# Optimization experiments

Hardware: AMD Instinct MI355X
Metric: run time of the kernel (lower is better)

## Reference

```python
import jax, jax.numpy as jnp
import numpy as np

B, S, F = 4, 2048, 512
H, DK, DV, FILT = 8, 64, 64, 512

def setup_inputs() -> dict:
    key = jax.random.key(0)
    ks = jax.random.split(key, 11)
    sc_in = 1.0 / np.sqrt(F)
    sc_o = 1.0 / np.sqrt(H * DV)
    return {
        "x_q": jax.random.normal(ks[0], (B, S, F), jnp.float32),
        "x_k": jax.random.normal(ks[1], (B, S, F), jnp.float32),
        "x_v": jax.random.normal(ks[2], (B, S, F), jnp.float32),
        "Wq": jax.random.normal(ks[3], (H, F, DK), jnp.float32) * sc_in,
        "bq": jax.random.normal(ks[4], (H, DK), jnp.float32) * 0.01,
        "Wk": jax.random.normal(ks[5], (H, F, DK), jnp.float32) * sc_in,
        "bk": jax.random.normal(ks[6], (H, DK), jnp.float32) * 0.01,
        "Wv": jax.random.normal(ks[7], (H, F, DV), jnp.float32) * sc_in,
        "bv": jax.random.normal(ks[8], (H, DV), jnp.float32) * 0.01,
        "Wo": jax.random.normal(ks[9], (H * DV, FILT), jnp.float32) * sc_o,
        "bo": jax.random.normal(ks[10], (FILT,), jnp.float32) * 0.01,
    }

def reference(x_q, x_k, x_v, Wq, bq, Wk, bk, Wv, bv, Wo, bo):
    d_k = Wq.shape[-1]
    # per-head Dense projections, batched over heads: [B,H,S,dk/dv]
    q = jnp.einsum("bsf,hfk->bhsk", x_q, Wq) + bq[:, None, :]
    k = jnp.einsum("bsf,hfk->bhsk", x_k, Wk) + bk[:, None, :]
    v = jnp.einsum("bsf,hfv->bhsv", x_v, Wv) + bv[:, None, :]
    # scaled dot-product attention (scale by 1/sqrt(d_k) as in map_fn)
    scores = jnp.einsum("bhsk,bhtk->bhst", q, k) / jnp.sqrt(jnp.asarray(d_k, q.dtype))
    attn = jax.nn.softmax(scores, axis=-1)
    out = jnp.einsum("bhst,bhtv->bhsv", attn, v)
    # concat heads along feature dim -> [B,S,H*DV], then output linear
    bsz, h, s, dv = out.shape
    concat = out.transpose(0, 2, 1, 3).reshape(bsz, s, h * dv)
    return concat @ Wo + bo
```

## Files before the change

kernel.cpp:

```cpp
#include <hip/hip_runtime.h>

#define B_    4
#define S_    2048
#define H_    8
#define M_    (B_ * S_)

typedef __bf16    bf16_t;
typedef _Float16  f16_t;
typedef __bf16   bf16x8 __attribute__((ext_vector_type(8)));
typedef __bf16   bf16x4 __attribute__((ext_vector_type(4)));
typedef _Float16 f16x8  __attribute__((ext_vector_type(8)));
typedef float    f32x16 __attribute__((ext_vector_type(16)));

union B8 { uint4 u; bf16x8 v; bf16_t e[8]; };
union B4 { uint2 u; bf16x4 v; bf16_t e[4]; };
union H8 { uint4 u; f16x8  v; f16_t  e[8]; };
union H4 { uint2 u; f16_t  e[4]; };

#define QSCALE 0.1803368801111204f

__global__ __launch_bounds__(256) void convert_weights(
    const float* __restrict__ w0, const float* __restrict__ w1,
    const float* __restrict__ w2, const float* __restrict__ wo,
    bf16_t* __restrict__ t0, bf16_t* __restrict__ t1,
    bf16_t* __restrict__ t2, f16_t* __restrict__ wot)
{
    __shared__ float T[64][65];
    const int z   = blockIdx.z;
    const int k0  = blockIdx.x * 64;
    const int tid = threadIdx.x;
    const int row = tid & 63, q4 = tid >> 6;

    if (z < 3) {
        const float* W  = z == 0 ? w0 : z == 1 ? w1 : w2;
        bf16_t*      Wt = z == 0 ? t0 : z == 1 ? t1 : t2;
        const int h = blockIdx.y;
        const float* Wh = W + (size_t)h * 512 * 64;
        #pragma unroll
        for (int i = 0; i < 4; ++i) {
            int fq = q4 * 4 + i;
            float4 v = *(const float4*)(Wh + (size_t)(k0 + row) * 64 + fq * 4);
            T[row][fq * 4 + 0] = v.x; T[row][fq * 4 + 1] = v.y;
            T[row][fq * 4 + 2] = v.z; T[row][fq * 4 + 3] = v.w;
        }
        __syncthreads();
        bf16_t* Wth = Wt + (size_t)h * 64 * 512;
        #pragma unroll
        for (int i = 0; i < 4; ++i) {
            int kq = q4 * 4 + i;
            B4 o;
            #pragma unroll
            for (int j = 0; j < 4; ++j) o.e[j] = (bf16_t)T[kq * 4 + j][row];
            *(uint2*)(Wth + (size_t)row * 512 + k0 + kq * 4) = o.u;
        }
    } else {
        const int n0 = blockIdx.y * 64;
        #pragma unroll
        for (int i = 0; i < 4; ++i) {
            int fq = q4 * 4 + i;
            float4 v = *(const float4*)(wo + (size_t)(k0 + row) * 512 + n0 + fq * 4);
            T[row][fq * 4 + 0] = v.x; T[row][fq * 4 + 1] = v.y;
            T[row][fq * 4 + 2] = v.z; T[row][fq * 4 + 3] = v.w;
        }
        __syncthreads();
        #pragma unroll
        for (int i = 0; i < 4; ++i) {
            int kq = q4 * 4 + i;
            H4 o;
            #pragma unroll
            for (int j = 0; j < 4; ++j) o.e[j] = (f16_t)T[kq * 4 + j][row];
            *(uint2*)(wot + (size_t)(n0 + row) * 512 + k0 + kq * 4) = o.u;
        }
    }
}

__global__ __launch_bounds__(256) void proj_tiled(
    const float* __restrict__ xq, const float* __restrict__ xk,
    const float* __restrict__ xv,
    const bf16_t* __restrict__ Wtq, const bf16_t* __restrict__ Wtk,
    const bf16_t* __restrict__ Wtv,
    const float* __restrict__ bq, const float* __restrict__ bk,
    const float* __restrict__ bv,
    bf16_t* __restrict__ Qb, bf16_t* __restrict__ Kb, bf16_t* __restrict__ Vt)
{
    __shared__ bf16_t As[128 * 72];
    __shared__ bf16_t Bs[128 * 72];

    const int z = blockIdx.z;
    const float*  X    = z == 0 ? xq  : z == 1 ? xk  : xv;
    const bf16_t* Wt   = z == 0 ? Wtq : z == 1 ? Wtk : Wtv;
    const float*  bias = z == 0 ? bq  : z == 1 ? bk  : bv;

    const int tid  = threadIdx.x;
    const int wave = tid >> 6, lane = tid & 63;
    const int l31  = lane & 31, half = lane >> 5;
    const int m0   = blockIdx.x * 128;
    const int n0   = blockIdx.y * 128;
    const int mw   = (wave & 1) * 64;
    const int nw   = (wave >> 1) * 64;

    const int sr = tid >> 1;
    const int sc = (tid & 1) * 32;

    float4 ra0[4], ra1[4];
    uint4  rb[4];
    {
        const float*  ap = X  + (size_t)(m0 + sr) * 512 + sc;
        const bf16_t* bp = Wt + (size_t)(n0 + sr) * 512 + sc;
        #pragma unroll
        for (int i = 0; i < 4; ++i) {
            ra0[i] = *(const float4*)(ap + i * 8);
            ra1[i] = *(const float4*)(ap + i * 8 + 4);
            rb[i]  = *(const uint4*)(bp + i * 8);
        }
    }

    f32x16 acc[2][2];
    #pragma unroll
    for (int mt = 0; mt < 2; ++mt)
        #pragma unroll
        for (int nt = 0; nt < 2; ++nt)
            #pragma unroll
            for (int i = 0; i < 16; ++i) acc[mt][nt][i] = 0.0f;

    for (int k0 = 0; k0 < 512; k0 += 64) {
        __syncthreads();
        #pragma unroll
        for (int i = 0; i < 4; ++i) {
            B8 w;
            w.e[0] = (bf16_t)ra0[i].x; w.e[1] = (bf16_t)ra0[i].y;
            w.e[2] = (bf16_t)ra0[i].z; w.e[3] = (bf16_t)ra0[i].w;
            w.e[4] = (bf16_t)ra1[i].x; w.e[5] = (bf16_t)ra1[i].y;
            w.e[6] = (bf16_t)ra1[i].z; w.e[7] = (bf16_t)ra1[i].w;
            *(uint4*)&As[sr * 72 + sc + i * 8] = w.u;
            *(uint4*)&Bs[sr * 72 + sc + i * 8] = rb[i];
        }
        __syncthreads();
        if (k0 + 64 < 512) {
            const float*  ap = X  + (size_t)(m0 + sr) * 512 + k0 + 64 + sc;
            const bf16_t* bp = Wt + (size_t)(n0 + sr) * 512 + k0 + 64 + sc;
            #pragma unroll
            for (int i = 0; i < 4; ++i) {
                ra0[i] = *(const float4*)(ap + i * 8);
                ra1[i] = *(const float4*)(ap + i * 8 + 4);
                rb[i]  = *(const uint4*)(bp + i * 8);
            }
        }

        #pragma unroll
        for (int kc = 0; kc < 4; ++kc) {
            B8 a0, a1, b0, b1;
            a0.u = *(const uint4*)&As[(mw + l31)      * 72 + kc * 16 + half * 8];
            a1.u = *(const uint4*)&As[(mw + 32 + l31) * 72 + kc * 16 + half * 8];
            b0.u = *(const uint4*)&Bs[(nw + l31)      * 72 + kc * 16 + half * 8];
            b1.u = *(const uint4*)&Bs[(nw + 32 + l31) * 72 + kc * 16 + half * 8];
            acc[0][0] = __builtin_amdgcn_mfma_f32_32x32x16_bf16(a0.v, b0.v, acc[0][0], 0, 0, 0);
            acc[0][1] = __builtin_amdgcn_mfma_f32_32x32x16_bf16(a0.v, b1.v, acc[0][1], 0, 0, 0);
            acc[1][0] = __builtin_amdgcn_mfma_f32_32x32x16_bf16(a1.v, b0.v, acc[1][0], 0, 0, 0);
            acc[1][1] = __builtin_amdgcn_mfma_f32_32x32x16_bf16(a1.v, b1.v, acc[1][1], 0, 0, 0);
        }
    }

    if (z <= 1) {
        const float sc_ = (z == 0) ? QSCALE : 1.0f;
        bf16_t* Out = (z == 0) ? Qb : Kb;
        #pragma unroll
        for (int mt = 0; mt < 2; ++mt)
            #pragma unroll
            for (int nt = 0; nt < 2; ++nt) {
                int n = n0 + nw + nt * 32 + l31;
                float bv_ = bias[n];
                #pragma unroll
                for (int r = 0; r < 16; ++r) {
                    int m = m0 + mw + mt * 32 + (r & 3) + 8 * (r >> 2) + 4 * half;
                    Out[(size_t)m * 512 + n] = (bf16_t)((acc[mt][nt][r] + bv_) * sc_);
                }
            }
    } else {
        const int b  = m0 >> 11;
        const int sb = (m0 & 2047);
        #pragma unroll
        for (int mt = 0; mt < 2; ++mt)
            #pragma unroll
            for (int nt = 0; nt < 2; ++nt) {
                int n = n0 + nw + nt * 32 + l31;
                float bv_ = bias[n];
                int h = n >> 6, d = n & 63;
                bf16_t* base = Vt + ((size_t)(b * 8 + h) * 64 + d) * 2048 + sb + mw + mt * 32;
                #pragma unroll
                for (int g = 0; g < 4; ++g) {
                    B4 p;
                    #pragma unroll
                    for (int j = 0; j < 4; ++j) p.e[j] = (bf16_t)(acc[mt][nt][g * 4 + j] + bv_);
                    *(uint2*)(base + 8 * g + 4 * half) = p.u;
                }
            }
    }
}

__global__ __launch_bounds__(512) void attn_mfma(
    const bf16_t* __restrict__ Q, const bf16_t* __restrict__ K,
    const bf16_t* __restrict__ Vt, f16_t* __restrict__ O)
{
    __shared__ char smraw[36864];
    bf16_t* KsBuf = (bf16_t*)smraw;
    bf16_t* VsBuf = KsBuf + 2 * 64 * 72;

    const int bh  = blockIdx.y;
    const int b   = bh >> 3, h = bh & 7;
    const int q0  = blockIdx.x * 128;
    const int tid = threadIdx.x;
    const int wave = tid >> 6, lane = tid & 63;
    const int l31 = lane & 31, half = lane >> 5;
    const int qsub = wave & 3, ksplit = wave >> 2;

    bf16x8 qf[4];
    {
        const bf16_t* qp = Q + ((size_t)(b * S_ + q0 + qsub * 32 + l31)) * 512 + h * 64 + half * 8;
        #pragma unroll
        for (int ks = 0; ks < 4; ++ks) {
            B8 t; t.u = *(const uint4*)(qp + ks * 16);
            qf[ks] = t.v;
        }
    }

    f32x16 o0, o1;
    #pragma unroll
    for (int i = 0; i < 16; ++i) { o0[i] = 0.0f; o1[i] = 0.0f; }
    float l_i = 0.0f;

    const bf16_t* Kbase = K + ((size_t)b * S_) * 512 + h * 64;
    const bf16_t* Vbase = Vt + ((size_t)bh * 64) * 2048;

    const int sbuf = tid >> 8;
    const int p    = tid & 255;
    const int kr = p >> 3, kc8 = p & 7;
    const int vd = p >> 2, vj = p & 3;
    const int kqmap[4] = {0, 2, 1, 3};
    const int vkq = kqmap[vj];
    bf16_t* KsS = KsBuf + sbuf * (64 * 72);
    bf16_t* VsS = VsBuf + sbuf * (64 * 72);
    const bf16_t* KsC = KsBuf + ksplit * (64 * 72);
    const bf16_t* VsC = VsBuf + ksplit * (64 * 72);

    uint4 kreg0, kreg1;
    uint2 vreg[4];
    {
        const int tb = sbuf * 1024;
        kreg0 = *(const uint4*)(Kbase + (size_t)(tb + kr) * 512 + kc8 * 8);
        kreg1 = *(const uint4*)(Kbase + (size_t)(tb + kr + 32) * 512 + kc8 * 8);
        #pragma unroll
        for (int g = 0; g < 4; ++g)
            vreg[g] = *(const uint2*)(Vbase + (size_t)vd * 2048 + tb + g * 16 + vkq * 4);
    }

    for (int t0 = 0; t0 < 1024; t0 += 64) {
        __syncthreads();
        *(uint4*)&KsS[kr * 72 + kc8 * 8]        = kreg0;
        *(uint4*)&KsS[(kr + 32) * 72 + kc8 * 8] = kreg1;
        #pragma unroll
        for (int g = 0; g < 4; ++g)
            *(uint2*)&VsS[vd * 72 + g * 16 + vj * 4] = vreg[g];
        __syncthreads();

        if (t0 + 64 < 1024) {
            const int tb = sbuf * 1024 + t0 + 64;
            kreg0 = *(const uint4*)(Kbase + (size_t)(tb + kr) * 512 + kc8 * 8);
            kreg1 = *(const uint4*)(Kbase + (size_t)(tb + kr + 32) * 512 + kc8 * 8);
            #pragma unroll
            for (int g = 0; g < 4; ++g)
                vreg[g] = *(const uint2*)(Vbase + (size_t)vd * 2048 + tb + g * 16 + vkq * 4);
        }

        f32x16 s0, s1;
        #pragma unroll
        for (int i = 0; i < 16; ++i) { s0[i] = 0.0f; s1[i] = 0.0f; }
        #pragma unroll
        for (int ks = 0; ks < 4; ++ks) {
            B8 k0, k1;
            k0.u = *(const uint4*)(&KsC[l31 * 72 + ks * 16 + half * 8]);
            k1.u = *(const uint4*)(&KsC[(32 + l31) * 72 + ks * 16 + half * 8]);
            s0 = __builtin_amdgcn_mfma_f32_32x32x16_bf16(k0.v, qf[ks], s0, 0, 0, 0);
            s1 = __builtin_amdgcn_mfma_f32_32x32x16_bf16(k1.v, qf[ks], s1, 0, 0, 0);
        }

        float ls = 0.0f;
        #pragma unroll
        for (int r = 0; r < 16; ++r) {
            s0[r] = __builtin_amdgcn_exp2f(s0[r]); ls += s0[r];
            s1[r] = __builtin_amdgcn_exp2f(s1[r]); ls += s1[r];
        }
        l_i += ls;

        B8 pf[4];
        #pragma unroll
        for (int j = 0; j < 8; ++j) {
            pf[0].e[j] = (bf16_t)s0[j];
            pf[1].e[j] = (bf16_t)s0[8 + j];
            pf[2].e[j] = (bf16_t)s1[j];
            pf[3].e[j] = (bf16_t)s1[8 + j];
        }

        #pragma unroll
        for (int c = 0; c < 4; ++c) {
            B8 va, vb;
            va.u = *(const uint4*)(&VsC[l31 * 72 + c * 16 + half * 8]);
            vb.u = *(const uint4*)(&VsC[(32 + l31) * 72 + c * 16 + half * 8]);
            o0 = __builtin_amdgcn_mfma_f32_32x32x16_bf16(va.v, pf[c].v, o0, 0, 0, 0);
            o1 = __builtin_amdgcn_mfma_f32_32x32x16_bf16(vb.v, pf[c].v, o1, 0, 0, 0);
        }
    }

    l_i += __shfl_xor(l_i, 32);
    __syncthreads();
    float* co = (float*)smraw;
    float* cl = co + 4 * 32 * 68;
    if (ksplit == 1) {
        float* reg = co + qsub * (32 * 68);
        #pragma unroll
        for (int r = 0; r < 16; ++r) {
            reg[r * 68 + lane]        = o0[r];
            reg[(16 + r) * 68 + lane] = o1[r];
        }
        cl[qsub * 64 + lane] = l_i;
    }
    __syncthreads();
    if (ksplit == 0) {
        float* reg = co + qsub * (32 * 68);
        float inv = 1.0f / (l_i + cl[qsub * 64 + lane]);
        f16_t* Ob = O + ((size_t)(b * S_ + q0 + qsub * 32 + l31)) * 512 + h * 64;
        #pragma unroll
        for (int g = 0; g < 4; ++g) {
            H4 a, c;
            #pragma unroll
            for (int j = 0; j < 4; ++j) {
                int r = g * 4 + j;
                a.e[j] = (f16_t)((o0[r] + reg[r * 68 + lane]) * inv);
                c.e[j] = (f16_t)((o1[r] + reg[(16 + r) * 68 + lane]) * inv);
            }
            int d = 8 * g + 4 * half;
            *(uint2*)(Ob + d)      = a.u;
            *(uint2*)(Ob + 32 + d) = c.u;
        }
    }
}

__global__ __launch_bounds__(256) void gemm_out_tiled(
    const f16_t* __restrict__ A, const f16_t* __restrict__ Wot,
    const float* __restrict__ bias, float* __restrict__ C)
{
    __shared__ f16_t As[64 * 72];
    __shared__ f16_t Bs[64 * 72];

    const int tid  = threadIdx.x;
    const int wave = tid >> 6, lane = tid & 63;
    const int l31  = lane & 31, half = lane >> 5;
    const int m0   = blockIdx.x * 64;
    const int n0   = blockIdx.y * 64;
    const int mw   = (wave & 1) * 32;
    const int nw   = (wave >> 1) * 32;

    const int sr  = tid >> 2;
    const int so  = (tid & 3) * 16;

    uint4 pA0, pA1, pB0, pB1;
    {
        const f16_t* ap = A   + (size_t)(m0 + sr) * 512 + so;
        const f16_t* bp = Wot + (size_t)(n0 + sr) * 512 + so;
        pA0 = *(const uint4*)(ap); pA1 = *(const uint4*)(ap + 8);
        pB0 = *(const uint4*)(bp); pB1 = *(const uint4*)(bp + 8);
    }

    f32x16 acc;
    #pragma unroll
    for (int i = 0; i < 16; ++i) acc[i] = 0.0f;

    for (int k0 = 0; k0 < 512; k0 += 64) {
        __syncthreads();
        *(uint4*)&As[sr * 72 + so]     = pA0;
        *(uint4*)&As[sr * 72 + so + 8] = pA1;
        *(uint4*)&Bs[sr * 72 + so]     = pB0;
        *(uint4*)&Bs[sr * 72 + so + 8] = pB1;
        __syncthreads();
        if (k0 + 64 < 512) {
            const f16_t* ap = A   + (size_t)(m0 + sr) * 512 + k0 + 64 + so;
            const f16_t* bp = Wot + (size_t)(n0 + sr) * 512 + k0 + 64 + so;
            pA0 = *(const uint4*)(ap); pA1 = *(const uint4*)(ap + 8);
            pB0 = *(const uint4*)(bp); pB1 = *(const uint4*)(bp + 8);
        }

        #pragma unroll
        for (int kc = 0; kc < 4; ++kc) {
            H8 a, b;
            a.u = *(const uint4*)&As[(mw + l31) * 72 + kc * 16 + half * 8];
            b.u = *(const uint4*)&Bs[(nw + l31) * 72 + kc * 16 + half * 8];
            acc = __builtin_amdgcn_mfma_f32_32x32x16_f16(a.v, b.v, acc, 0, 0, 0);
        }
    }

    const int n = n0 + nw + l31;
    const float bias0 = bias[n];
    #pragma unroll
    for (int r = 0; r < 16; ++r) {
        int m = m0 + mw + (r & 3) + 8 * (r >> 2) + 4 * half;
        C[(size_t)m * 512 + n] = acc[r] + bias0;
    }
}

extern "C" void kernel_launch(void* const* d_in, const int* in_sizes, int n_in,
                              void* d_out, int out_size, void* d_ws, size_t ws_size,
                              hipStream_t stream)
{
    const float* x_q = (const float*)d_in[0];
    const float* x_k = (const float*)d_in[1];
    const float* x_v = (const float*)d_in[2];
    const float* Wq  = (const float*)d_in[3];
    const float* bq  = (const float*)d_in[4];
    const float* Wk  = (const float*)d_in[5];
    const float* bk  = (const float*)d_in[6];
    const float* Wv  = (const float*)d_in[7];
    const float* bv  = (const float*)d_in[8];
    const float* Wo  = (const float*)d_in[9];
    const float* bo  = (const float*)d_in[10];
    float* out = (float*)d_out;

    char* W = (char*)d_ws;
    bf16_t* Wtq = (bf16_t*)W;
    bf16_t* Wtk = Wtq + (size_t)8 * 64 * 512;
    bf16_t* Wtv = Wtk + (size_t)8 * 64 * 512;
    f16_t*  Wot = (f16_t*)(Wtv + (size_t)8 * 64 * 512);
    bf16_t* Qb  = (bf16_t*)(Wot + (size_t)512 * 512);
    bf16_t* Kb  = Qb + (size_t)M_ * 512;
    bf16_t* Vt  = Kb + (size_t)M_ * 512;
    f16_t*  AO  = (f16_t*)(Vt + (size_t)M_ * 512);

    convert_weights<<<dim3(8, 8, 4), 256, 0, stream>>>(
        Wq, Wk, Wv, Wo, Wtq, Wtk, Wtv, Wot);

    proj_tiled<<<dim3(64, 4, 3), 256, 0, stream>>>(
        x_q, x_k, x_v, Wtq, Wtk, Wtv, bq, bk, bv, Qb, Kb, Vt);

    attn_mfma<<<dim3(S_ / 128, B_ * H_), 512, 0, stream>>>(Qb, Kb, Vt, AO);

    gemm_out_tiled<<<dim3(128, 8), 256, 0, stream>>>(AO, Wot, bo, out);
}
```

Before: 214.5 us.

## Fuse weight transpose and conversion into projection and output GEMM loaders

Removes the separate convert_weights kernel and instead reads fp32 weights directly inside the projection and output GEMMs, converting to bf16/f16 in registers and scattering them transposed into shared memory. This saves a kernel launch and the workspace round trip for the converted weights. In exchange each GEMM block repeats the weight conversion, reads twice as many weight bytes as fp32, and does scalar 2-byte shared-memory stores that may bank-conflict. The pipeline was also reordered so the next-tile global loads are issued before the second barrier.

After: 223.5 us. 1.04x slower.

```diff
diff --git a/kernel.cpp b/kernel.cpp
--- a/kernel.cpp
+++ b/kernel.cpp
@@ -19,66 +19,20 @@
 
 #define QSCALE 0.1803368801111204f
 
-__global__ __launch_bounds__(256) void convert_weights(
-    const float* __restrict__ w0, const float* __restrict__ w1,
-    const float* __restrict__ w2, const float* __restrict__ wo,
-    bf16_t* __restrict__ t0, bf16_t* __restrict__ t1,
-    bf16_t* __restrict__ t2, f16_t* __restrict__ wot)
-{
-    __shared__ float T[64][65];
-    const int z   = blockIdx.z;
-    const int k0  = blockIdx.x * 64;
-    const int tid = threadIdx.x;
-    const int row = tid & 63, q4 = tid >> 6;
-
-    if (z < 3) {
-        const float* W  = z == 0 ? w0 : z == 1 ? w1 : w2;
-        bf16_t*      Wt = z == 0 ? t0 : z == 1 ? t1 : t2;
-        const int h = blockIdx.y;
-        const float* Wh = W + (size_t)h * 512 * 64;
-        #pragma unroll
-        for (int i = 0; i < 4; ++i) {
-            int fq = q4 * 4 + i;
-            float4 v = *(const float4*)(Wh + (size_t)(k0 + row) * 64 + fq * 4);
-            T[row][fq * 4 + 0] = v.x; T[row][fq * 4 + 1] = v.y;
-            T[row][fq * 4 + 2] = v.z; T[row][fq * 4 + 3] = v.w;
-        }
-        __syncthreads();
-        bf16_t* Wth = Wt + (size_t)h * 64 * 512;
-        #pragma unroll
-        for (int i = 0; i < 4; ++i) {
-            int kq = q4 * 4 + i;
-            B4 o;
-            #pragma unroll
-            for (int j = 0; j < 4; ++j) o.e[j] = (bf16_t)T[kq * 4 + j][row];
-            *(uint2*)(Wth + (size_t)row * 512 + k0 + kq * 4) = o.u;
-        }
-    } else {
-        const int n0 = blockIdx.y * 64;
-        #pragma unroll
-        for (int i = 0; i < 4; ++i) {
-            int fq = q4 * 4 + i;
-            float4 v = *(const float4*)(wo + (size_t)(k0 + row) * 512 + n0 + fq * 4);
-            T[row][fq * 4 + 0] = v.x; T[row][fq * 4 + 1] = v.y;
-            T[row][fq * 4 + 2] = v.z; T[row][fq * 4 + 3] = v.w;
-        }
-        __syncthreads();
-        #pragma unroll
-        for (int i = 0; i < 4; ++i) {
-            int kq = q4 * 4 + i;
-            H4 o;
-            #pragma unroll
-            for (int j = 0; j < 4; ++j) o.e[j] = (f16_t)T[kq * 4 + j][row];
-            *(uint2*)(wot + (size_t)(n0 + row) * 512 + k0 + kq * 4) = o.u;
-        }
-    }
+__device__ __forceinline__ uint4 pack_bf16x8(float4 a, float4 b) {
+    B8 w;
+    w.e[0] = (bf16_t)a.x; w.e[1] = (bf16_t)a.y;
+    w.e[2] = (bf16_t)a.z; w.e[3] = (bf16_t)a.w;
+    w.e[4] = (bf16_t)b.x; w.e[5] = (bf16_t)b.y;
+    w.e[6] = (bf16_t)b.z; w.e[7] = (bf16_t)b.w;
+    return w.u;
 }
 
 __global__ __launch_bounds__(256) void proj_tiled(
     const float* __restrict__ xq, const float* __restrict__ xk,
     const float* __restrict__ xv,
-    const bf16_t* __restrict__ Wtq, const bf16_t* __restrict__ Wtk,
-    const bf16_t* __restrict__ Wtv,
+    const float* __restrict__ Wq, const float* __restrict__ Wk,
+    const float* __restrict__ Wv,
     const float* __restrict__ bq, const float* __restrict__ bk,
     const float* __restrict__ bv,
     bf16_t* __restrict__ Qb, bf16_t* __restrict__ Kb, bf16_t* __restrict__ Vt)
@@ -87,9 +41,9 @@
     __shared__ bf16_t Bs[128 * 72];
 
     const int z = blockIdx.z;
-    const float*  X    = z == 0 ? xq  : z == 1 ? xk  : xv;
-    const bf16_t* Wt   = z == 0 ? Wtq : z == 1 ? Wtk : Wtv;
-    const float*  bias = z == 0 ? bq  : z == 1 ? bk  : bv;
+    const float* X    = z == 0 ? xq : z == 1 ? xk : xv;
+    const float* Wsrc = z == 0 ? Wq : z == 1 ? Wk : Wv;
+    const float* bias = z == 0 ? bq : z == 1 ? bk : bv;
 
     const int tid  = threadIdx.x;
     const int wave = tid >> 6, lane = tid & 63;
@@ -101,17 +55,35 @@
 
     const int sr = tid >> 1;
     const int sc = (tid & 1) * 32;
-
-    float4 ra0[4], ra1[4];
-    uint4  rb[4];
+    const int kk  = tid & 63;
+    const int oct = tid >> 6;
+    size_t wbase[4];
+    int    nloc[4];
+    #pragma unroll
+    for (int r4 = 0; r4 < 4; ++r4) {
+        int nl = (oct + r4 * 4) * 8;
+        nloc[r4] = nl;
+        int h = (n0 + nl) >> 6;
+        wbase[r4] = ((size_t)h * 512 + kk) * 64 + ((n0 + nl) & 63);
+    }
+
+    uint4 ab[4];
+    B4 pw0[4], pw1[4];
     {
-        const float*  ap = X  + (size_t)(m0 + sr) * 512 + sc;
-        const bf16_t* bp = Wt + (size_t)(n0 + sr) * 512 + sc;
-        #pragma unroll
-        for (int i = 0; i < 4; ++i) {
-            ra0[i] = *(const float4*)(ap + i * 8);
-            ra1[i] = *(const float4*)(ap + i * 8 + 4);
-            rb[i]  = *(const uint4*)(bp + i * 8);
+        const float* ap = X + (size_t)(m0 + sr) * 512 + sc;
+        #pragma unroll
+        for (int i = 0; i < 4; ++i)
+            ab[i] = pack_bf16x8(*(const float4*)(ap + i * 8),
+                                *(const float4*)(ap + i * 8 + 4));
+        #pragma unroll
+        for (int r4 = 0; r4 < 4; ++r4) {
+            const float* wp = Wsrc + wbase[r4];
+            float4 a = *(const float4*)(wp);
+            float4 b = *(const float4*)(wp + 4);
+            pw0[r4].e[0] = (bf16_t)a.x; pw0[r4].e[1] = (bf16_t)a.y;
+            pw0[r4].e[2] = (bf16_t)a.z; pw0[r4].e[3] = (bf16_t)a.w;
+            pw1[r4].e[0] = (bf16_t)b.x; pw1[r4].e[1] = (bf16_t)b.y;
+            pw1[r4].e[2] = (bf16_t)b.z; pw1[r4].e[3] = (bf16_t)b.w;
         }
     }
 
@@ -126,26 +98,34 @@
     for (int k0 = 0; k0 < 512; k0 += 64) {
         __syncthreads();
         #pragma unroll
-        for (int i = 0; i < 4; ++i) {
-            B8 w;
-            w.e[0] = (bf16_t)ra0[i].x; w.e[1] = (bf16_t)ra0[i].y;
-            w.e[2] = (bf16_t)ra0[i].z; w.e[3] = (bf16_t)ra0[i].w;
-            w.e[4] = (bf16_t)ra1[i].x; w.e[5] = (bf16_t)ra1[i].y;
-            w.e[6] = (bf16_t)ra1[i].z; w.e[7] = (bf16_t)ra1[i].w;
-            *(uint4*)&As[sr * 72 + sc + i * 8] = w.u;
-            *(uint4*)&Bs[sr * 72 + sc + i * 8] = rb[i];
-        }
-        __syncthreads();
+        for (int i = 0; i < 4; ++i)
+            *(uint4*)&As[sr * 72 + sc + i * 8] = ab[i];
+        #pragma unroll
+        for (int r4 = 0; r4 < 4; ++r4) {
+            #pragma unroll
+            for (int j = 0; j < 4; ++j) {
+                Bs[(nloc[r4] + j) * 72 + kk]     = pw0[r4].e[j];
+                Bs[(nloc[r4] + 4 + j) * 72 + kk] = pw1[r4].e[j];
+            }
+        }
         if (k0 + 64 < 512) {
-            const float*  ap = X  + (size_t)(m0 + sr) * 512 + k0 + 64 + sc;
-            const bf16_t* bp = Wt + (size_t)(n0 + sr) * 512 + k0 + 64 + sc;
-            #pragma unroll
-            for (int i = 0; i < 4; ++i) {
-                ra0[i] = *(const float4*)(ap + i * 8);
-                ra1[i] = *(const float4*)(ap + i * 8 + 4);
-                rb[i]  = *(const uint4*)(bp + i * 8);
-            }
-        }
+            const float* ap = X + (size_t)(m0 + sr) * 512 + k0 + 64 + sc;
+            #pragma unroll
+            for (int i = 0; i < 4; ++i)
+                ab[i] = pack_bf16x8(*(const float4*)(ap + i * 8),
+                                    *(const float4*)(ap + i * 8 + 4));
+            #pragma unroll
+            for (int r4 = 0; r4 < 4; ++r4) {
+                const float* wp = Wsrc + wbase[r4] + (size_t)(k0 + 64) * 64;
+                float4 a = *(const float4*)(wp);
+                float4 b = *(const float4*)(wp + 4);
+                pw0[r4].e[0] = (bf16_t)a.x; pw0[r4].e[1] = (bf16_t)a.y;
+                pw0[r4].e[2] = (bf16_t)a.z; pw0[r4].e[3] = (bf16_t)a.w;
+                pw1[r4].e[0] = (bf16_t)b.x; pw1[r4].e[1] = (bf16_t)b.y;
+                pw1[r4].e[2] = (bf16_t)b.z; pw1[r4].e[3] = (bf16_t)b.w;
+            }
+        }
+        __syncthreads();
 
         #pragma unroll
         for (int kc = 0; kc < 4; ++kc) {
@@ -346,7 +326,7 @@
 }
 
 __global__ __launch_bounds__(256) void gemm_out_tiled(
-    const f16_t* __restrict__ A, const f16_t* __restrict__ Wot,
+    const f16_t* __restrict__ A, const float* __restrict__ Wo,
     const float* __restrict__ bias, float* __restrict__ C)
 {
     __shared__ f16_t As[64 * 72];
@@ -360,15 +340,29 @@
     const int mw   = (wave & 1) * 32;
     const int nw   = (wave >> 1) * 32;
 
-    const int sr  = tid >> 2;
-    const int so  = (tid & 3) * 16;
-
-    uint4 pA0, pA1, pB0, pB1;
+    const int sr = tid >> 2;
+    const int so = (tid & 3) * 16;
+    const int kk  = tid & 63;
+    const int oct = tid >> 6;
+    int nloc[2];
+    nloc[0] = oct * 8;
+    nloc[1] = (oct + 4) * 8;
+
+    uint4 pA0, pA1;
+    H4 pw0[2], pw1[2];
     {
-        const f16_t* ap = A   + (size_t)(m0 + sr) * 512 + so;
-        const f16_t* bp = Wot + (size_t)(n0 + sr) * 512 + so;
+        const f16_t* ap = A + (size_t)(m0 + sr) * 512 + so;
         pA0 = *(const uint4*)(ap); pA1 = *(const uint4*)(ap + 8);
-        pB0 = *(const uint4*)(bp); pB1 = *(const uint4*)(bp + 8);
+        #pragma unroll
+        for (int r2 = 0; r2 < 2; ++r2) {
+            const float* wp = Wo + (size_t)kk * 512 + n0 + nloc[r2];
+            float4 a = *(const float4*)(wp);
+            float4 b = *(const float4*)(wp + 4);
+            pw0[r2].e[0] = (f16_t)a.x; pw0[r2].e[1] = (f16_t)a.y;
+            pw0[r2].e[2] = (f16_t)a.z; pw0[r2].e[3] = (f16_t)a.w;
+            pw1[r2].e[0] = (f16_t)b.x; pw1[r2].e[1] = (f16_t)b.y;
+            pw1[r2].e[2] = (f16_t)b.z; pw1[r2].e[3] = (f16_t)b.w;
+        }
     }
 
     f32x16 acc;
@@ -379,15 +373,29 @@
         __syncthreads();
         *(uint4*)&As[sr * 72 + so]     = pA0;
         *(uint4*)&As[sr * 72 + so + 8] = pA1;
-        *(uint4*)&Bs[sr * 72 + so]     = pB0;
-        *(uint4*)&Bs[sr * 72 + so + 8] = pB1;
-        __syncthreads();
+        #pragma unroll
+        for (int r2 = 0; r2 < 2; ++r2) {
+            #pragma unroll
+            for (int j = 0; j < 4; ++j) {
+                Bs[(nloc[r2] + j) * 72 + kk]     = pw0[r2].e[j];
+                Bs[(nloc[r2] + 4 + j) * 72 + kk] = pw1[r2].e[j];
+            }
+        }
         if (k0 + 64 < 512) {
-            const f16_t* ap = A   + (size_t)(m0 + sr) * 512 + k0 + 64 + so;
-            const f16_t* bp = Wot + (size_t)(n0 + sr) * 512 + k0 + 64 + so;
+            const f16_t* ap = A + (size_t)(m0 + sr) * 512 + k0 + 64 + so;
             pA0 = *(const uint4*)(ap); pA1 = *(const uint4*)(ap + 8);
-            pB0 = *(const uint4*)(bp); pB1 = *(const uint4*)(bp + 8);
-        }
+            #pragma unroll
+            for (int r2 = 0; r2 < 2; ++r2) {
+                const float* wp = Wo + (size_t)(k0 + 64 + kk) * 512 + n0 + nloc[r2];
+                float4 a = *(const float4*)(wp);
+                float4 b = *(const float4*)(wp + 4);
+                pw0[r2].e[0] = (f16_t)a.x; pw0[r2].e[1] = (f16_t)a.y;
+                pw0[r2].e[2] = (f16_t)a.z; pw0[r2].e[3] = (f16_t)a.w;
+                pw1[r2].e[0] = (f16_t)b.x; pw1[r2].e[1] = (f16_t)b.y;
+                pw1[r2].e[2] = (f16_t)b.z; pw1[r2].e[3] = (f16_t)b.w;
+            }
+        }
+        __syncthreads();
 
         #pragma unroll
         for (int kc = 0; kc < 4; ++kc) {
@@ -424,23 +432,15 @@
     const float* bo  = (const float*)d_in[10];
     float* out = (float*)d_out;
 
-    char* W = (char*)d_ws;
-    bf16_t* Wtq = (bf16_t*)W;
-    bf16_t* Wtk = Wtq + (size_t)8 * 64 * 512;
-    bf16_t* Wtv = Wtk + (size_t)8 * 64 * 512;
-    f16_t*  Wot = (f16_t*)(Wtv + (size_t)8 * 64 * 512);
-    bf16_t* Qb  = (bf16_t*)(Wot + (size_t)512 * 512);
-    bf16_t* Kb  = Qb + (size_t)M_ * 512;
-    bf16_t* Vt  = Kb + (size_t)M_ * 512;
-    f16_t*  AO  = (f16_t*)(Vt + (size_t)M_ * 512);
-
-    convert_weights<<<dim3(8, 8, 4), 256, 0, stream>>>(
-        Wq, Wk, Wv, Wo, Wtq, Wtk, Wtv, Wot);
+    bf16_t* Qb = (bf16_t*)d_ws;
+    bf16_t* Kb = Qb + (size_t)M_ * 512;
+    bf16_t* Vt = Kb + (size_t)M_ * 512;
+    f16_t*  AO = (f16_t*)(Vt + (size_t)M_ * 512);
 
     proj_tiled<<<dim3(64, 4, 3), 256, 0, stream>>>(
-        x_q, x_k, x_v, Wtq, Wtk, Wtv, bq, bk, bv, Qb, Kb, Vt);
+        x_q, x_k, x_v, Wq, Wk, Wv, bq, bk, bv, Qb, Kb, Vt);
 
     attn_mfma<<<dim3(S_ / 128, B_ * H_), 512, 0, stream>>>(Qb, Kb, Vt, AO);
 
-    gemm_out_tiled<<<dim3(128, 8), 256, 0, stream>>>(AO, Wot, bo, out);
+    gemm_out_tiled<<<dim3(128, 8), 256, 0, stream>>>(AO, Wo, bo, out);
 }
```

## Split projection GEMM K-dimension across two wave groups with LDS reduction

Applied to the files above, without the earlier changes.

The QKV projection kernel now runs 512 threads per block, with two groups of four waves each handling half of the 512-wide K dimension in separate LDS buffers. The partial accumulators are then summed through shared memory before the epilogue. The global prefetch for the next K step is also moved before the barrier, so it overlaps more with the MMA work. The aim is more waves in flight per block to hide load latency in this small-K GEMM, at the cost of doubled LDS use (72KB) and an extra reduction pass through shared memory.

After: 233.1 us. +8.7%, slower.

```diff
diff --git a/kernel.cpp b/kernel.cpp
--- a/kernel.cpp
+++ b/kernel.cpp
@@ -18,6 +18,15 @@
 union H4 { uint2 u; f16_t  e[4]; };
 
 #define QSCALE 0.1803368801111204f
+
+__device__ __forceinline__ uint4 pack_bf16x8(float4 a, float4 b) {
+    B8 w;
+    w.e[0] = (bf16_t)a.x; w.e[1] = (bf16_t)a.y;
+    w.e[2] = (bf16_t)a.z; w.e[3] = (bf16_t)a.w;
+    w.e[4] = (bf16_t)b.x; w.e[5] = (bf16_t)b.y;
+    w.e[6] = (bf16_t)b.z; w.e[7] = (bf16_t)b.w;
+    return w.u;
+}
 
 __global__ __launch_bounds__(256) void convert_weights(
     const float* __restrict__ w0, const float* __restrict__ w1,
@@ -74,7 +83,7 @@
     }
 }
 
-__global__ __launch_bounds__(256) void proj_tiled(
+__global__ __launch_bounds__(512, 4) void proj_split(
     const float* __restrict__ xq, const float* __restrict__ xk,
     const float* __restrict__ xv,
     const bf16_t* __restrict__ Wtq, const bf16_t* __restrict__ Wtk,
@@ -83,8 +92,9 @@
     const float* __restrict__ bv,
     bf16_t* __restrict__ Qb, bf16_t* __restrict__ Kb, bf16_t* __restrict__ Vt)
 {
-    __shared__ bf16_t As[128 * 72];
-    __shared__ bf16_t Bs[128 * 72];
+    __shared__ char smraw[73728];
+    bf16_t* As = (bf16_t*)smraw;
+    bf16_t* Bs = (bf16_t*)(smraw + 36864);
 
     const int z = blockIdx.z;
     const float*  X    = z == 0 ? xq  : z == 1 ? xk  : xv;
@@ -94,25 +104,28 @@
     const int tid  = threadIdx.x;
     const int wave = tid >> 6, lane = tid & 63;
     const int l31  = lane & 31, half = lane >> 5;
+    const int wq   = wave & 3, ksp = wave >> 2;
     const int m0   = blockIdx.x * 128;
     const int n0   = blockIdx.y * 128;
-    const int mw   = (wave & 1) * 64;
-    const int nw   = (wave >> 1) * 64;
-
-    const int sr = tid >> 1;
-    const int sc = (tid & 1) * 32;
+    const int mw   = (wq & 1) * 64;
+    const int nw   = (wq >> 1) * 64;
+
+    const int p  = tid & 255;
+    const int sr = p >> 1;
+    const int sc = (p & 1) * 32;
+    bf16_t* AsS = As + ksp * (128 * 72);
+    bf16_t* BsS = Bs + ksp * (128 * 72);
+
+    const float*  Abase = X  + (size_t)(m0 + sr) * 512 + ksp * 256 + sc;
+    const bf16_t* Bbase = Wt + (size_t)(n0 + sr) * 512 + ksp * 256 + sc;
 
     float4 ra0[4], ra1[4];
     uint4  rb[4];
-    {
-        const float*  ap = X  + (size_t)(m0 + sr) * 512 + sc;
-        const bf16_t* bp = Wt + (size_t)(n0 + sr) * 512 + sc;
-        #pragma unroll
-        for (int i = 0; i < 4; ++i) {
-            ra0[i] = *(const float4*)(ap + i * 8);
-            ra1[i] = *(const float4*)(ap + i * 8 + 4);
-            rb[i]  = *(const uint4*)(bp + i * 8);
-        }
+    #pragma unroll
+    for (int i = 0; i < 4; ++i) {
+        ra0[i] = *(const float4*)(Abase + i * 8);
+        ra1[i] = *(const float4*)(Abase + i * 8 + 4);
+        rb[i]  = *(const uint4*)(Bbase + i * 8);
     }
 
     f32x16 acc[2][2];
@@ -123,22 +136,16 @@
             #pragma unroll
             for (int i = 0; i < 16; ++i) acc[mt][nt][i] = 0.0f;
 
-    for (int k0 = 0; k0 < 512; k0 += 64) {
+    for (int k0 = 0; k0 < 256; k0 += 64) {
         __syncthreads();
         #pragma unroll
         for (int i = 0; i < 4; ++i) {
-            B8 w;
-            w.e[0] = (bf16_t)ra0[i].x; w.e[1] = (bf16_t)ra0[i].y;
-            w.e[2] = (bf16_t)ra0[i].z; w.e[3] = (bf16_t)ra0[i].w;
-            w.e[4] = (bf16_t)ra1[i].x; w.e[5] = (bf16_t)ra1[i].y;
-            w.e[6] = (bf16_t)ra1[i].z; w.e[7] = (bf16_t)ra1[i].w;
-            *(uint4*)&As[sr * 72 + sc + i * 8] = w.u;
-            *(uint4*)&Bs[sr * 72 + sc + i * 8] = rb[i];
-        }
-        __syncthreads();
-        if (k0 + 64 < 512) {
-            const float*  ap = X  + (size_t)(m0 + sr) * 512 + k0 + 64 + sc;
-            const bf16_t* bp = Wt + (size_t)(n0 + sr) * 512 + k0 + 64 + sc;
+            *(uint4*)&AsS[sr * 72 + sc + i * 8] = pack_bf16x8(ra0[i], ra1[i]);
+            *(uint4*)&BsS[sr * 72 + sc + i * 8] = rb[i];
+        }
+        if (k0 + 64 < 256) {
+            const float*  ap = Abase + k0 + 64;
+            const bf16_t* bp = Bbase + k0 + 64;
             #pragma unroll
             for (int i = 0; i < 4; ++i) {
                 ra0[i] = *(const float4*)(ap + i * 8);
@@ -146,19 +153,48 @@
                 rb[i]  = *(const uint4*)(bp + i * 8);
             }
         }
-
+        __syncthreads();
+
+        const bf16_t* AsC = As + ksp * (128 * 72);
+        const bf16_t* BsC = Bs + ksp * (128 * 72);
         #pragma unroll
         for (int kc = 0; kc < 4; ++kc) {
             B8 a0, a1, b0, b1;
-            a0.u = *(const uint4*)&As[(mw + l31)      * 72 + kc * 16 + half * 8];
-            a1.u = *(const uint4*)&As[(mw + 32 + l31) * 72 + kc * 16 + half * 8];
-            b0.u = *(const uint4*)&Bs[(nw + l31)      * 72 + kc * 16 + half * 8];
-            b1.u = *(const uint4*)&Bs[(nw + 32 + l31) * 72 + kc * 16 + half * 8];
+            a0.u = *(const uint4*)&AsC[(mw + l31)      * 72 + kc * 16 + half * 8];
+            a1.u = *(const uint4*)&AsC[(mw + 32 + l31) * 72 + kc * 16 + half * 8];
+            b0.u = *(const uint4*)&BsC[(nw + l31)      * 72 + kc * 16 + half * 8];
+            b1.u = *(const uint4*)&BsC[(nw + 32 + l31) * 72 + kc * 16 + half * 8];
             acc[0][0] = __builtin_amdgcn_mfma_f32_32x32x16_bf16(a0.v, b0.v, acc[0][0], 0, 0, 0);
             acc[0][1] = __builtin_amdgcn_mfma_f32_32x32x16_bf16(a0.v, b1.v, acc[0][1], 0, 0, 0);
             acc[1][0] = __builtin_amdgcn_mfma_f32_32x32x16_bf16(a1.v, b0.v, acc[1][0], 0, 0, 0);
             acc[1][1] = __builtin_amdgcn_mfma_f32_32x32x16_bf16(a1.v, b1.v, acc[1][1], 0, 0, 0);
         }
+    }
+
+    __syncthreads();
+    float* comb = (float*)smraw;
+    if (ksp == 1) {
+        float* reg = comb + wq * 4096;
+        #pragma unroll
+        for (int mt = 0; mt < 2; ++mt)
+            #pragma unroll
+            for (int nt = 0; nt < 2; ++nt)
+                #pragma unroll
+                for (int r = 0; r < 16; ++r)
+                    reg[((mt * 2 + nt) * 16 + r) * 64 + lane] = acc[mt][nt][r];
+    }
+    __syncthreads();
+    if (ksp != 0) return;
+
+    {
+        float* reg = comb + wq * 4096;
+        #pragma unroll
+        for (int mt = 0; mt < 2; ++mt)
+            #pragma unroll
+            for (int nt = 0; nt < 2; ++nt)
+                #pragma unroll
+                for (int r = 0; r < 16; ++r)
+                    acc[mt][nt][r] += reg[((mt * 2 + nt) * 16 + r) * 64 + lane];
     }
 
     if (z <= 1) {
@@ -189,10 +225,10 @@
                 bf16_t* base = Vt + ((size_t)(b * 8 + h) * 64 + d) * 2048 + sb + mw + mt * 32;
                 #pragma unroll
                 for (int g = 0; g < 4; ++g) {
-                    B4 p;
+                    B4 pk;
                     #pragma unroll
-                    for (int j = 0; j < 4; ++j) p.e[j] = (bf16_t)(acc[mt][nt][g * 4 + j] + bv_);
-                    *(uint2*)(base + 8 * g + 4 * half) = p.u;
+                    for (int j = 0; j < 4; ++j) pk.e[j] = (bf16_t)(acc[mt][nt][g * 4 + j] + bv_);
+                    *(uint2*)(base + 8 * g + 4 * half) = pk.u;
                 }
             }
     }
@@ -437,7 +473,7 @@
     convert_weights<<<dim3(8, 8, 4), 256, 0, stream>>>(
         Wq, Wk, Wv, Wo, Wtq, Wtk, Wtv, Wot);
 
-    proj_tiled<<<dim3(64, 4, 3), 256, 0, stream>>>(
+    proj_split<<<dim3(64, 4, 3), 512, 0, stream>>>(
         x_q, x_k, x_v, Wtq, Wtk, Wtv, bq, bk, bv, Qb, Kb, Vt);
 
     attn_mfma<<<dim3(S_ / 128, B_ * H_), 512, 0, stream>>>(Qb, Kb, Vt, AO);
```
